# Optimization experiments

Measured on AMD Instinct MI355X. Metric: run time of the kernel, lower is better.

The kernel has to match this reference:

```python
import jax, jax.numpy as jnp
import numpy as np

N_NODES = 100000
N_EDGES = 1600000
N_GRAPHS = 512
HIDDEN = 128
N_CLASSES = 10


def setup_inputs() -> dict:
    key = jax.random.key(0)
    ks = jax.random.split(key, 12)
    edge_index = jax.random.randint(ks[0], (2, N_EDGES), 0, N_NODES, dtype=jnp.int32)
    batch = jnp.sort(jax.random.randint(ks[1], (N_NODES,), 0, N_GRAPHS, dtype=jnp.int32))
    def lin(k, fi, fo):
        return jax.random.normal(k, (fi, fo), jnp.float32) * (1.0 / np.sqrt(fi))
    return {
        "edge_index": edge_index,
        "batch": batch,
        "W0": lin(ks[2], 1, HIDDEN),
        "b0": jax.random.normal(ks[3], (HIDDEN,), jnp.float32) * 0.01,
        "W1": lin(ks[4], HIDDEN, HIDDEN),
        "b1": jax.random.normal(ks[5], (HIDDEN,), jnp.float32) * 0.01,
        "W2": lin(ks[6], HIDDEN, HIDDEN),
        "b2": jax.random.normal(ks[7], (HIDDEN,), jnp.float32) * 0.01,
        "Wp": lin(ks[8], HIDDEN, N_CLASSES),
        "bp": jax.random.normal(ks[9], (N_CLASSES,), jnp.float32) * 0.01,
    }


def _gcn_setup(edge_index, n_nodes):
    # add self-loops (PyG GCNConv default) and compute symmetric normalization
    loop = jnp.arange(n_nodes, dtype=edge_index.dtype)
    src = jnp.concatenate([edge_index[0], loop])  # [E+N]
    dst = jnp.concatenate([edge_index[1], loop])
    deg = jax.ops.segment_sum(jnp.ones_like(src, dtype=jnp.float32), dst,
                              num_segments=n_nodes)
    dinv = jnp.where(deg > 0, jax.lax.rsqrt(deg), 0.0)
    norm = dinv[src] * dinv[dst]  # [E+N]
    return src, dst, norm


def _gcn_conv(x, W, b, src, dst, norm, n_nodes):
    h = x @ W                                # [N, out]
    msg = h[src] * norm[:, None]             # gather + scale, [E+N, out]
    out = jax.ops.segment_sum(msg, dst, num_segments=n_nodes)
    return out + b


def reference(edge_index, batch, W0, b0, W1, b1, W2, b2, Wp, bp):
    n = batch.shape[0]
    src, dst, norm = _gcn_setup(edge_index, n)
    x = jnp.ones((n, 1), jnp.float32)  # forward() hardcodes ones as features
    for W, b in ((W0, b0), (W1, b1), (W2, b2)):
        x = jax.nn.relu(_gcn_conv(x, W, b, src, dst, norm, n))
        # dropout_p = 0.0 -> identity
    # scatter_mean pooling over graphs
    s = jax.ops.segment_sum(x, batch, num_segments=N_GRAPHS)
    cnt = jax.ops.segment_sum(jnp.ones((n,), jnp.float32), batch,
                              num_segments=N_GRAPHS)
    pooled = s / jnp.maximum(cnt, 1.0)[:, None]
    logits = pooled @ Wp + bp
    return jax.nn.log_softmax(logits, axis=1)
```

## Files before the change

kernel.cpp:

```cpp
#include <hip/hip_runtime.h>

#define HID 128
#define NG 512
#define NC 10
#define SCHUNK 512
#define BSH 9
#define TILE 4096

typedef unsigned int u32;
typedef unsigned short u16;
typedef __attribute__((ext_vector_type(8))) short short8;
typedef __attribute__((ext_vector_type(4))) float f32x4;

static __device__ __forceinline__ int gtid() {
    return blockIdx.x * blockDim.x + threadIdx.x;
}

static __device__ __forceinline__ u16 f2bf(float f) {
    u32 u = __float_as_uint(f);
    u32 r = u + 0x7fffu + ((u >> 16) & 1u);
    return (u16)(r >> 16);
}
static __device__ __forceinline__ float bf2f(u32 s) {
    return __uint_as_float(s << 16);
}
static __device__ __forceinline__ void bf8_unpack(uint4 u, float* f) {
    f[0] = bf2f(u.x & 0xffffu); f[1] = bf2f(u.x >> 16);
    f[2] = bf2f(u.y & 0xffffu); f[3] = bf2f(u.y >> 16);
    f[4] = bf2f(u.z & 0xffffu); f[5] = bf2f(u.z >> 16);
    f[6] = bf2f(u.w & 0xffffu); f[7] = bf2f(u.w >> 16);
}


__global__ void k_hist(const int* __restrict__ dst, int* __restrict__ cnt, int E) {
    int i = gtid();
    if (i < E) atomicAdd(&cnt[dst[i]], 1);
}

__global__ __launch_bounds__(256) void k_scan1(const int* __restrict__ cnt,
                                               int* __restrict__ partial, int N) {
    __shared__ int s[256];
    int t = threadIdx.x;
    int i0 = blockIdx.x * SCHUNK + t * 2;
    int v = 0;
    if (i0 < N) v += cnt[i0];
    if (i0 + 1 < N) v += cnt[i0 + 1];
    s[t] = v;
    __syncthreads();
    for (int off = 128; off > 0; off >>= 1) {
        if (t < off) s[t] += s[t + off];
        __syncthreads();
    }
    if (t == 0) partial[blockIdx.x] = s[0];
}

__global__ __launch_bounds__(256) void k_scan2(int* __restrict__ partial, int B) {
    __shared__ int s[256];
    int t = threadIdx.x;
    int own = (t < B) ? partial[t] : 0;
    s[t] = own;
    __syncthreads();
    for (int off = 1; off < 256; off <<= 1) {
        int v = (t >= off) ? s[t - off] : 0;
        __syncthreads();
        s[t] += v;
        __syncthreads();
    }
    if (t < B) partial[t] = s[t] - own;
}

__global__ __launch_bounds__(256) void k_scan3(const int* __restrict__ cnt,
                                               const int* __restrict__ partial,
                                               int* __restrict__ rowptr,
                                               float* __restrict__ dinv, int N) {
    __shared__ int s[256];
    int t = threadIdx.x;
    int i0 = blockIdx.x * SCHUNK + t * 2;
    int c0 = 0, c1 = 0;
    if (i0 < N) c0 = cnt[i0];
    if (i0 + 1 < N) c1 = cnt[i0 + 1];
    int own = c0 + c1;
    s[t] = own;
    __syncthreads();
    for (int off = 1; off < 256; off <<= 1) {
        int v = (t >= off) ? s[t - off] : 0;
        __syncthreads();
        s[t] += v;
        __syncthreads();
    }
    int base = partial[blockIdx.x] + s[t] - own;
    if (i0 < N) { rowptr[i0] = base; dinv[i0] = rsqrtf(1.0f + (float)c0); }
    if (i0 + 1 < N) { rowptr[i0 + 1] = base + c0; dinv[i0 + 1] = rsqrtf(1.0f + (float)c1); }
    if (i0 >= N - 2 && i0 < N) rowptr[N] = base + own;
}


__global__ void k_binit(const int* __restrict__ rowptr, int* __restrict__ bcur, int NB) {
    int b = gtid();
    if (b < NB) bcur[b] = rowptr[b << BSH];
}

__global__ __launch_bounds__(256) void k_part1(const int* __restrict__ src,
                                               const int* __restrict__ dst,
                                               int* __restrict__ bcur,
                                               uint2* __restrict__ tmp, int E, int NB) {
    __shared__ int cnt[256];
    __shared__ int base[256];
    int t = threadIdx.x;
    int e0 = blockIdx.x * TILE;
    for (int i = t; i < NB; i += 256) cnt[i] = 0;
    __syncthreads();
    int s_[16], d_[16];
#pragma unroll
    for (int k = 0; k < 16; ++k) {
        int e = e0 + k * 256 + t;
        if (e < E) {
            s_[k] = src[e];
            d_[k] = dst[e];
            atomicAdd(&cnt[d_[k] >> BSH], 1);
        } else {
            d_[k] = -1;
        }
    }
    __syncthreads();
    for (int i = t; i < NB; i += 256) {
        base[i] = atomicAdd(&bcur[i], cnt[i]);
        cnt[i] = 0;
    }
    __syncthreads();
#pragma unroll
    for (int k = 0; k < 16; ++k) {
        if (d_[k] >= 0) {
            int b = d_[k] >> BSH;
            int pos = base[b] + atomicAdd(&cnt[b], 1);
            tmp[pos] = make_uint2((u32)s_[k], (u32)d_[k]);
        }
    }
}

__global__ __launch_bounds__(512) void k_part2(const int* __restrict__ rowptr,
                                               const uint2* __restrict__ tmp,
                                               u32* __restrict__ packed, int N) {
    __shared__ int cur[1 << BSH];
    int b = blockIdx.x;
    int v0 = b << BSH;
    int nv = N - v0; if (nv > (1 << BSH)) nv = 1 << BSH;
    int t = threadIdx.x;
    for (int i = t; i < nv; i += 512) cur[i] = rowptr[v0 + i];
    __syncthreads();
    int e0 = rowptr[v0];
    int vend = v0 + nv;
    int e1 = rowptr[vend];
    for (int e = e0 + t; e < e1; e += 512) {
        uint2 p = tmp[e];
        int pos = atomicAdd(&cur[p.y & ((1 << BSH) - 1)], 1);
        packed[pos] = p.x;
    }
}

__global__ __launch_bounds__(256) void k_sl0(const int* __restrict__ rowptr,
                                             const u32* __restrict__ packed,
                                             const float* __restrict__ dinv,
                                             const float* __restrict__ W0,
                                             const float* __restrict__ b0,
                                             u16* __restrict__ x, int N) {
    int lane = threadIdx.x & 31;
    int v = (blockIdx.x * 256 + threadIdx.x) >> 5;
    if (v >= N) return;
    int r0 = rowptr[v], r1 = rowptr[v + 1];
    float s = 0.0f;
    for (int j = r0 + lane; j < r1; j += 32) s += dinv[packed[j]];
#pragma unroll
    for (int off = 16; off > 0; off >>= 1) s += __shfl_xor(s, off, 32);
    float di = dinv[v];
    s = di * (di + s);
    int d0 = lane * 4;
    float4 w = *(const float4*)&W0[d0];
    float4 b = *(const float4*)&b0[d0];
    float a0 = fmaxf(fmaf(s, w.x, b.x), 0.0f);
    float a1 = fmaxf(fmaf(s, w.y, b.y), 0.0f);
    float a2 = fmaxf(fmaf(s, w.z, b.z), 0.0f);
    float a3 = fmaxf(fmaf(s, w.w, b.w), 0.0f);
    uint2 o;
    o.x = (u32)f2bf(a0) | ((u32)f2bf(a1) << 16);
    o.y = (u32)f2bf(a2) | ((u32)f2bf(a3) << 16);
    *(uint2*)&x[(size_t)v * HID + d0] = o;
}

__global__ __launch_bounds__(256) void k_wt(const float* __restrict__ W,
                                            u16* __restrict__ Wt) {
    int t = gtid();
    if (t >= 2048) return;
    int n = t >> 4;
    int j = t & 15;
    int js = j ^ (n & 7);
    u32 w0 = (u32)f2bf(W[(j * 8 + 0) * HID + n]) | ((u32)f2bf(W[(j * 8 + 1) * HID + n]) << 16);
    u32 w1 = (u32)f2bf(W[(j * 8 + 2) * HID + n]) | ((u32)f2bf(W[(j * 8 + 3) * HID + n]) << 16);
    u32 w2 = (u32)f2bf(W[(j * 8 + 4) * HID + n]) | ((u32)f2bf(W[(j * 8 + 5) * HID + n]) << 16);
    u32 w3 = (u32)f2bf(W[(j * 8 + 6) * HID + n]) | ((u32)f2bf(W[(j * 8 + 7) * HID + n]) << 16);
    uint4 o = make_uint4(w0, w1, w2, w3);
    *(uint4*)&Wt[(size_t)n * HID + js * 8] = o;
}

__global__ __launch_bounds__(256) void k_gemm(const u16* __restrict__ x,
                                              const u16* __restrict__ Wt,
                                              const float* __restrict__ dinv,
                                              u16* __restrict__ q, int nrows) {
    __shared__ u16 Wl[HID * HID];
    int tid = threadIdx.x;
    for (int i = tid; i < 2048; i += 256)
        *(uint4*)&Wl[i * 8] = *(const uint4*)&Wt[i * 8];

    int w = tid >> 6;
    int l = tid & 63;
    int R0 = blockIdx.x * 64 + w * 16;
    int arow = R0 + (l & 15);
    int koff = (l >> 4) * 8;

    short8 a[4];
#pragma unroll
    for (int kb = 0; kb < 4; ++kb) {
        if (arow < nrows)
            a[kb] = *(const short8*)&x[(size_t)arow * HID + kb * 32 + koff];
        else
            a[kb] = (short8)0;
    }
    __syncthreads();

    int colbase = l & 15;
    int rowq = (l >> 4) * 4;
    float dv[4];
#pragma unroll
    for (int i = 0; i < 4; ++i) {
        int orow = R0 + rowq + i;
        dv[i] = (orow < nrows) ? dinv[orow] : 0.0f;
    }
#pragma unroll
    for (int cb = 0; cb < 8; ++cb) {
        f32x4 acc = {0.0f, 0.0f, 0.0f, 0.0f};
        int wrow = cb * 16 + (l & 15);
#pragma unroll
        for (int kb = 0; kb < 4; ++kb) {
            int j = (kb * 4 + (l >> 4)) ^ (wrow & 7);
            short8 b = *(const short8*)&Wl[wrow * HID + j * 8];
            acc = __builtin_amdgcn_mfma_f32_16x16x32_bf16(a[kb], b, acc, 0, 0, 0);
        }
#pragma unroll
        for (int i = 0; i < 4; ++i) {
            int orow = R0 + rowq + i;
            if (orow < nrows)
                q[(size_t)orow * HID + cb * 16 + colbase] = f2bf(acc[i] * dv[i]);
        }
    }
}

__global__ __launch_bounds__(256) void k_aggr(const u32* __restrict__ packed,
                                              const int* __restrict__ rowptr,
                                              const u16* __restrict__ q,
                                              const float* __restrict__ dinv,
                                              const float* __restrict__ b,
                                              u16* __restrict__ y, int N) {
    int lane = threadIdx.x & 31;
    int v = (blockIdx.x * 256 + threadIdx.x) >> 5;
    if (v >= N) return;
    int r0 = rowptr[v], r1 = rowptr[v + 1];
    int half = lane >> 4;
    int d8 = (lane & 15) * 8;

    float acc[8];
    if (half == 0) {
        uint4 qv = *(const uint4*)&q[(size_t)v * HID + d8];
        bf8_unpack(qv, acc);
    } else {
#pragma unroll
        for (int j = 0; j < 8; ++j) acc[j] = 0.0f;
    }

    for (int base = r0; base < r1; base += 32) {
        int idx = base + lane;
        u32 e = (idx < r1) ? packed[idx] : 0xFFFFFFFFu;
        int m = r1 - base; if (m > 32) m = 32;
        int iters = (m + 1) >> 1;
        for (int k = 0; k < iters; ++k) {
            u32 s = __shfl(e, 2 * k + half, 32);
            if (s != 0xFFFFFFFFu) {
                uint4 hq = *(const uint4*)&q[(size_t)s * HID + d8];
                float f[8];
                bf8_unpack(hq, f);
#pragma unroll
                for (int j = 0; j < 8; ++j) acc[j] += f[j];
            }
        }
    }
#pragma unroll
    for (int j = 0; j < 8; ++j) acc[j] += __shfl_xor(acc[j], 16, 32);

    if (half == 0) {
        float dv = dinv[v];
        float4 b0 = *(const float4*)&b[d8];
        float4 b1 = *(const float4*)&b[d8 + 4];
        float o[8];
        o[0] = fmaxf(fmaf(acc[0], dv, b0.x), 0.0f);
        o[1] = fmaxf(fmaf(acc[1], dv, b0.y), 0.0f);
        o[2] = fmaxf(fmaf(acc[2], dv, b0.z), 0.0f);
        o[3] = fmaxf(fmaf(acc[3], dv, b0.w), 0.0f);
        o[4] = fmaxf(fmaf(acc[4], dv, b1.x), 0.0f);
        o[5] = fmaxf(fmaf(acc[5], dv, b1.y), 0.0f);
        o[6] = fmaxf(fmaf(acc[6], dv, b1.z), 0.0f);
        o[7] = fmaxf(fmaf(acc[7], dv, b1.w), 0.0f);
        uint4 u;
        u.x = (u32)f2bf(o[0]) | ((u32)f2bf(o[1]) << 16);
        u.y = (u32)f2bf(o[2]) | ((u32)f2bf(o[3]) << 16);
        u.z = (u32)f2bf(o[4]) | ((u32)f2bf(o[5]) << 16);
        u.w = (u32)f2bf(o[6]) | ((u32)f2bf(o[7]) << 16);
        *(uint4*)&y[(size_t)v * HID + d8] = u;
    }
}


__global__ void k_pool(const u16* __restrict__ x, const int* __restrict__ batch,
                       float* __restrict__ pooled, float* __restrict__ cnt, int N) {
    const int K = 32;
    int d = threadIdx.x & (HID - 1);
    int chunk = blockIdx.x * 2 + (threadIdx.x >> 7);
    int v0 = chunk * K;
    if (v0 >= N) return;
    int vend = v0 + K; if (vend > N) vend = N;
    int g = batch[v0];
    float acc = 0.0f, c = 0.0f;
    for (int v = v0; v < vend; ++v) {
        int gv = batch[v];
        if (gv != g) {
            atomicAdd(&pooled[g * HID + d], acc);
            if (d == 0) atomicAdd(&cnt[g], c);
            acc = 0.0f; c = 0.0f; g = gv;
        }
        acc += bf2f((u32)x[(size_t)v * HID + d]);
        c += 1.0f;
    }
    atomicAdd(&pooled[g * HID + d], acc);
    if (d == 0) atomicAdd(&cnt[g], c);
}

__global__ void k_head(const float* __restrict__ pooled, const float* __restrict__ cnt,
                       const float* __restrict__ Wp, const float* __restrict__ bp,
                       float* __restrict__ out) {
    int g = gtid();
    if (g >= NG) return;
    float inv = 1.0f / fmaxf(cnt[g], 1.0f);
    float l[NC];
#pragma unroll
    for (int c = 0; c < NC; ++c) l[c] = bp[c];
    for (int d = 0; d < HID; ++d) {
        float pv = pooled[g * HID + d] * inv;
#pragma unroll
        for (int c = 0; c < NC; ++c) l[c] = fmaf(pv, Wp[d * NC + c], l[c]);
    }
    float m = l[0];
#pragma unroll
    for (int c = 1; c < NC; ++c) m = fmaxf(m, l[c]);
    float s = 0.0f;
#pragma unroll
    for (int c = 0; c < NC; ++c) s += expf(l[c] - m);
    float ls = logf(s) + m;
#pragma unroll
    for (int c = 0; c < NC; ++c) out[g * NC + c] = l[c] - ls;
}

extern "C" void kernel_launch(void* const* d_in, const int* in_sizes, int n_in,
                              void* d_out, int out_size, void* d_ws, size_t ws_size,
                              hipStream_t stream) {
    const int* ei    = (const int*)d_in[0];
    int E            = in_sizes[0] / 2;
    const int* src   = ei;
    const int* dstp  = ei + E;
    const int* batch = (const int*)d_in[1];
    int N            = in_sizes[1];
    const float* W0  = (const float*)d_in[2];
    const float* b0  = (const float*)d_in[3];
    const float* W1  = (const float*)d_in[4];
    const float* b1  = (const float*)d_in[5];
    const float* W2  = (const float*)d_in[6];
    const float* b2  = (const float*)d_in[7];
    const float* Wp  = (const float*)d_in[8];
    const float* bp  = (const float*)d_in[9];
    float* out       = (float*)d_out;

    u16*  xA     = (u16*)d_ws;
    u16*  xB     = xA + (size_t)N * HID;
    u32*  packed = (u32*)(xB + (size_t)N * HID);
    uint2* tmp   = (uint2*)(packed + E);
    u16*  Wt1    = (u16*)(tmp + E);
    u16*  Wt2    = Wt1 + HID * HID;
    int*  cnt_i  = (int*)(Wt2 + HID * HID);
    int*  rowptr = cnt_i + N;
    int*  bcur   = rowptr + N + 1;
    int*  partial= bcur + 256;
    float* dinv  = (float*)(partial + 256);
    float* pooled= dinv + N;
    float* cntg  = pooled + NG * HID;

    auto cdiv = [](int a, int b) { return (a + b - 1) / b; };
    int B  = cdiv(N, SCHUNK);
    int NB = cdiv(N, 1 << BSH);

    hipMemsetAsync(cnt_i, 0, N * sizeof(int), stream);
    hipMemsetAsync(pooled, 0, (NG * HID + NG) * sizeof(float), stream);

    k_hist<<<cdiv(E, 256), 256, 0, stream>>>(dstp, cnt_i, E);
    k_scan1<<<B, 256, 0, stream>>>(cnt_i, partial, N);
    k_scan2<<<1, 256, 0, stream>>>(partial, B);
    k_scan3<<<B, 256, 0, stream>>>(cnt_i, partial, rowptr, dinv, N);

    k_binit<<<1, 256, 0, stream>>>(rowptr, bcur, NB);
    k_part1<<<cdiv(E, TILE), 256, 0, stream>>>(src, dstp, bcur, tmp, E, NB);
    k_part2<<<NB, 512, 0, stream>>>(rowptr, tmp, packed, N);

    k_wt<<<8, 256, 0, stream>>>(W1, Wt1);
    k_wt<<<8, 256, 0, stream>>>(W2, Wt2);

    k_sl0<<<cdiv(N, 8), 256, 0, stream>>>(rowptr, packed, dinv, W0, b0, xA, N);

    k_gemm<<<cdiv(N, 64), 256, 0, stream>>>(xA, Wt1, dinv, xB, N);
    k_aggr<<<cdiv(N, 8), 256, 0, stream>>>(packed, rowptr, xB, dinv, b1, xA, N);

    k_gemm<<<cdiv(N, 64), 256, 0, stream>>>(xA, Wt2, dinv, xB, N);
    k_aggr<<<cdiv(N, 8), 256, 0, stream>>>(packed, rowptr, xB, dinv, b2, xA, N);

    k_pool<<<cdiv(cdiv(N, 32), 2), 256, 0, stream>>>(xA, batch, pooled, cntg, N);
    k_head<<<2, 256, 0, stream>>>(pooled, cntg, Wp, bp, out);
}
```

Before: 333.1 us.

## Build CSR from bucket histogram and compute per-node offsets inside part2

Replaces the per-node global atomic histogram and three-pass scan with a bucket-level histogram using shared-memory atomics plus a single-block scan of bucket counts. Per-node counts, rowptr and dinv are now computed inside k_part2 through a block-local histogram and scan over each bucket's edges. This removes the 1.6M global atomics, the N-sized memset and several kernel launches. In exchange, k_part2 reads tmp twice and does an extra shared-memory scan per bucket.

```diff
diff --git a/kernel.cpp b/kernel.cpp
--- a/kernel.cpp
+++ b/kernel.cpp
@@ -3,8 +3,8 @@
 #define HID 128
 #define NG 512
 #define NC 10
-#define SCHUNK 512
 #define BSH 9
+#define BSZ (1 << BSH)
 #define TILE 4096
 
 typedef unsigned int u32;
@@ -31,33 +31,29 @@
     f[6] = bf2f(u.w & 0xffffu); f[7] = bf2f(u.w >> 16);
 }
 
-
-__global__ void k_hist(const int* __restrict__ dst, int* __restrict__ cnt, int E) {
-    int i = gtid();
-    if (i < E) atomicAdd(&cnt[dst[i]], 1);
-}
-
-__global__ __launch_bounds__(256) void k_scan1(const int* __restrict__ cnt,
-                                               int* __restrict__ partial, int N) {
+__global__ __launch_bounds__(256) void k_bhist(const int* __restrict__ dst,
+                                               int* __restrict__ bcnt, int E, int NB) {
+    __shared__ int cnt[256];
+    int t = threadIdx.x;
+    int e0 = blockIdx.x * TILE;
+    for (int i = t; i < NB; i += 256) cnt[i] = 0;
+    __syncthreads();
+#pragma unroll
+    for (int k = 0; k < 16; ++k) {
+        int e = e0 + k * 256 + t;
+        if (e < E) atomicAdd(&cnt[dst[e] >> BSH], 1);
+    }
+    __syncthreads();
+    for (int i = t; i < NB; i += 256)
+        if (cnt[i] > 0) atomicAdd(&bcnt[i], cnt[i]);
+}
+
+__global__ __launch_bounds__(256) void k_bscan(const int* __restrict__ bcnt,
+                                               int* __restrict__ bbase,
+                                               int* __restrict__ bcur, int NB, int E) {
     __shared__ int s[256];
     int t = threadIdx.x;
-    int i0 = blockIdx.x * SCHUNK + t * 2;
-    int v = 0;
-    if (i0 < N) v += cnt[i0];
-    if (i0 + 1 < N) v += cnt[i0 + 1];
-    s[t] = v;
-    __syncthreads();
-    for (int off = 128; off > 0; off >>= 1) {
-        if (t < off) s[t] += s[t + off];
-        __syncthreads();
-    }
-    if (t == 0) partial[blockIdx.x] = s[0];
-}
-
-__global__ __launch_bounds__(256) void k_scan2(int* __restrict__ partial, int B) {
-    __shared__ int s[256];
-    int t = threadIdx.x;
-    int own = (t < B) ? partial[t] : 0;
+    int own = (t < NB) ? bcnt[t] : 0;
     s[t] = own;
     __syncthreads();
     for (int off = 1; off < 256; off <<= 1) {
@@ -66,38 +62,12 @@
         s[t] += v;
         __syncthreads();
     }
-    if (t < B) partial[t] = s[t] - own;
-}
-
-__global__ __launch_bounds__(256) void k_scan3(const int* __restrict__ cnt,
-                                               const int* __restrict__ partial,
-                                               int* __restrict__ rowptr,
-                                               float* __restrict__ dinv, int N) {
-    __shared__ int s[256];
-    int t = threadIdx.x;
-    int i0 = blockIdx.x * SCHUNK + t * 2;
-    int c0 = 0, c1 = 0;
-    if (i0 < N) c0 = cnt[i0];
-    if (i0 + 1 < N) c1 = cnt[i0 + 1];
-    int own = c0 + c1;
-    s[t] = own;
-    __syncthreads();
-    for (int off = 1; off < 256; off <<= 1) {
-        int v = (t >= off) ? s[t - off] : 0;
-        __syncthreads();
-        s[t] += v;
-        __syncthreads();
-    }
-    int base = partial[blockIdx.x] + s[t] - own;
-    if (i0 < N) { rowptr[i0] = base; dinv[i0] = rsqrtf(1.0f + (float)c0); }
-    if (i0 + 1 < N) { rowptr[i0 + 1] = base + c0; dinv[i0 + 1] = rsqrtf(1.0f + (float)c1); }
-    if (i0 >= N - 2 && i0 < N) rowptr[N] = base + own;
-}
-
-
-__global__ void k_binit(const int* __restrict__ rowptr, int* __restrict__ bcur, int NB) {
-    int b = gtid();
-    if (b < NB) bcur[b] = rowptr[b << BSH];
+    if (t < NB) {
+        int b = s[t] - own;
+        bbase[t] = b;
+        bcur[t] = b;
+    }
+    if (t == 0) bbase[NB] = E;
 }
 
 __global__ __launch_bounds__(256) void k_part1(const int* __restrict__ src,
@@ -124,7 +94,7 @@
     }
     __syncthreads();
     for (int i = t; i < NB; i += 256) {
-        base[i] = atomicAdd(&bcur[i], cnt[i]);
+        if (cnt[i] > 0) base[i] = atomicAdd(&bcur[i], cnt[i]);
         cnt[i] = 0;
     }
     __syncthreads();
@@ -138,22 +108,46 @@
     }
 }
 
-__global__ __launch_bounds__(512) void k_part2(const int* __restrict__ rowptr,
+__global__ __launch_bounds__(512) void k_part2(const int* __restrict__ bbase,
                                                const uint2* __restrict__ tmp,
-                                               u32* __restrict__ packed, int N) {
-    __shared__ int cur[1 << BSH];
+                                               u32* __restrict__ packed,
+                                               int* __restrict__ rowptr,
+                                               float* __restrict__ dinv,
+                                               int N, int NB) {
+    __shared__ int cnt[BSZ];
+    __shared__ int scn[BSZ];
+    __shared__ int cur[BSZ];
     int b = blockIdx.x;
     int v0 = b << BSH;
-    int nv = N - v0; if (nv > (1 << BSH)) nv = 1 << BSH;
+    int nv = N - v0; if (nv > BSZ) nv = BSZ;
     int t = threadIdx.x;
-    for (int i = t; i < nv; i += 512) cur[i] = rowptr[v0 + i];
-    __syncthreads();
-    int e0 = rowptr[v0];
-    int vend = v0 + nv;
-    int e1 = rowptr[vend];
+    int e0 = bbase[b], e1 = bbase[b + 1];
+
+    cnt[t] = 0;
+    __syncthreads();
+    for (int e = e0 + t; e < e1; e += 512)
+        atomicAdd(&cnt[tmp[e].y & (BSZ - 1)], 1);
+    __syncthreads();
+    int own = cnt[t];
+    scn[t] = own;
+    __syncthreads();
+    for (int off = 1; off < BSZ; off <<= 1) {
+        int v = (t >= off) ? scn[t - off] : 0;
+        __syncthreads();
+        scn[t] += v;
+        __syncthreads();
+    }
+    int start = e0 + scn[t] - own;
+    cur[t] = start;
+    if (t < nv) {
+        rowptr[v0 + t] = start;
+        dinv[v0 + t] = rsqrtf(1.0f + (float)own);
+    }
+    if (b == NB - 1 && t == 0) rowptr[N] = e1;
+    __syncthreads();
     for (int e = e0 + t; e < e1; e += 512) {
         uint2 p = tmp[e];
-        int pos = atomicAdd(&cur[p.y & ((1 << BSH) - 1)], 1);
+        int pos = atomicAdd(&cur[p.y & (BSZ - 1)], 1);
         packed[pos] = p.x;
     }
 }
@@ -392,29 +386,24 @@
     uint2* tmp   = (uint2*)(packed + E);
     u16*  Wt1    = (u16*)(tmp + E);
     u16*  Wt2    = Wt1 + HID * HID;
-    int*  cnt_i  = (int*)(Wt2 + HID * HID);
-    int*  rowptr = cnt_i + N;
-    int*  bcur   = rowptr + N + 1;
-    int*  partial= bcur + 256;
-    float* dinv  = (float*)(partial + 256);
+    int*  rowptr = (int*)(Wt2 + HID * HID);
+    int*  bcnt   = rowptr + N + 1;
+    int*  bbase  = bcnt + 256;
+    int*  bcur   = bbase + 257;
+    float* dinv  = (float*)(bcur + 256);
     float* pooled= dinv + N;
     float* cntg  = pooled + NG * HID;
 
     auto cdiv = [](int a, int b) { return (a + b - 1) / b; };
-    int B  = cdiv(N, SCHUNK);
-    int NB = cdiv(N, 1 << BSH);
-
-    hipMemsetAsync(cnt_i, 0, N * sizeof(int), stream);
+    int NB = cdiv(N, BSZ);
+
+    hipMemsetAsync(bcnt, 0, 256 * sizeof(int), stream);
     hipMemsetAsync(pooled, 0, (NG * HID + NG) * sizeof(float), stream);
 
-    k_hist<<<cdiv(E, 256), 256, 0, stream>>>(dstp, cnt_i, E);
-    k_scan1<<<B, 256, 0, stream>>>(cnt_i, partial, N);
-    k_scan2<<<1, 256, 0, stream>>>(partial, B);
-    k_scan3<<<B, 256, 0, stream>>>(cnt_i, partial, rowptr, dinv, N);
-
-    k_binit<<<1, 256, 0, stream>>>(rowptr, bcur, NB);
+    k_bhist<<<cdiv(E, TILE), 256, 0, stream>>>(dstp, bcnt, E, NB);
+    k_bscan<<<1, 256, 0, stream>>>(bcnt, bbase, bcur, NB, E);
     k_part1<<<cdiv(E, TILE), 256, 0, stream>>>(src, dstp, bcur, tmp, E, NB);
-    k_part2<<<NB, 512, 0, stream>>>(rowptr, tmp, packed, N);
+    k_part2<<<NB, 512, 0, stream>>>(bbase, tmp, packed, rowptr, dinv, N, NB);
 
     k_wt<<<8, 256, 0, stream>>>(W1, Wt1);
     k_wt<<<8, 256, 0, stream>>>(W2, Wt2);
```

Result: faster. 281.4 us (-15.5%).
